# Kernel optimization log

Hardware: AMD Instinct MI355X
Metric: run time of the kernel (lower is better)

## Reference

```python
import jax, jax.numpy as jnp
import numpy as np

HEADS = 16
D_K = 64  # hidden_size // heads = 1024 // 16
SCALE = D_K ** 0.5


def setup_inputs() -> dict:
    key = jax.random.key(0)
    ks = jax.random.split(key, 7)
    B, S, D = 4, 2048, 1024
    H = 1024  # hidden_size
    O = 1024  # outputs_dims
    s = 0.02
    return {
        "query": jax.random.normal(ks[0], (B, S, D), dtype=jnp.float32),
        "key": jax.random.normal(ks[1], (B, S, D), dtype=jnp.float32),
        "value": jax.random.normal(ks[2], (B, S, D), dtype=jnp.float32),
        "Wq": jax.random.normal(ks[3], (D, H), dtype=jnp.float32) * s,
        "Wk": jax.random.normal(ks[4], (D, H), dtype=jnp.float32) * s,
        "Wv": jax.random.normal(ks[5], (D, H), dtype=jnp.float32) * s,
        "Wo": jax.random.normal(ks[6], (H, O), dtype=jnp.float32) * s,
    }


def reference(query, key, value, Wq, Wk, Wv, Wo):
    B, S, _ = query.shape
    # Dense projections with relu activation (as in the original module)
    q = jax.nn.relu(query @ Wq).reshape(B, S, HEADS, D_K)  # [B,S,H,dk]
    k = jax.nn.relu(key @ Wk).reshape(B, S, HEADS, D_K)
    v = jax.nn.relu(value @ Wv).reshape(B, S, HEADS, D_K)
    # scores: [B,H,Sq,Sk]
    scores = jnp.einsum('bqhd,bkhd->bhqk', q, k) / SCALE
    attn = jax.nn.softmax(scores, axis=-1)
    # attention-weighted values -> [B,Sq,H,dk] -> [B,Sq,H*dk]
    ctx = jnp.einsum('bhqk,bkhd->bqhd', attn, v).reshape(B, S, HEADS * D_K)
    out = jax.nn.relu(ctx @ Wo)
    return out
```

## Files before the change

kernel.cpp:

```cpp
#include <hip/hip_runtime.h>

typedef unsigned short u16;
typedef __bf16 bf16x8 __attribute__((ext_vector_type(8)));
typedef float f32x4 __attribute__((ext_vector_type(4)));
typedef u16 u16x8 __attribute__((ext_vector_type(8)));
typedef u16 u16x4 __attribute__((ext_vector_type(4)));

#define MFMA16(a, b, c) __builtin_amdgcn_mfma_f32_16x16x32_bf16(a, b, c, 0, 0, 0)

static constexpr float QSC = 0.18033688011112042f;

__device__ inline u16 f2bf(float f) {
  union { float f; unsigned u; } x; x.f = f;
  unsigned r = x.u + 0x7FFF + ((x.u >> 16) & 1);
  return (u16)(r >> 16);
}
__device__ inline u16 cvt_bf(float f) {
  __bf16 h = (__bf16)f; return __builtin_bit_cast(u16, h);
}
__device__ inline bf16x8 ld_frag(const u16* p) {
  return __builtin_bit_cast(bf16x8, *(const u16x8*)p);
}
__device__ inline void dma16(const u16* g, u16* l) {
  __builtin_amdgcn_global_load_lds(
      (const __attribute__((address_space(1))) unsigned*)g,
      (__attribute__((address_space(3))) unsigned*)l, 16, 0, 0);
}

#if __has_builtin(__builtin_amdgcn_exp2f)
#define EXP2(x) __builtin_amdgcn_exp2f(x)
#else
#define EXP2(x) exp2f(x)
#endif

__launch_bounds__(256)
__global__ void prep_w(const float* __restrict__ Wq, const float* __restrict__ Wk,
                       const float* __restrict__ Wv, const float* __restrict__ Wo,
                       u16* __restrict__ Wt) {
  __shared__ u16 T[64 * 72];
  const int z = blockIdx.z;
  const float* W = z == 0 ? Wq : z == 1 ? Wk : z == 2 ? Wv : Wo;
  u16* D = Wt + ((size_t)z << 20);
  const int k0 = blockIdx.y * 64, c0 = blockIdx.x * 64;
  const int tid = threadIdx.x;
  const int kr = tid >> 2, cs = (tid & 3) * 16;
  const float* src = W + (size_t)(k0 + kr) * 1024 + c0 + cs;
  float f[16];
#pragma unroll
  for (int i = 0; i < 4; ++i) *(float4*)&f[i * 4] = ((const float4*)src)[i];
#pragma unroll
  for (int i = 0; i < 16; ++i) T[(cs + i) * 72 + kr] = cvt_bf(f[i]);
  __syncthreads();
  const int nn = tid >> 2, ks = (tid & 3) * 16;
  u16* dst = D + (size_t)(c0 + nn) * 1024 + k0 + ks;
  *(u16x8*)dst = *(u16x8*)&T[nn * 72 + ks];
  *(u16x8*)(dst + 8) = *(u16x8*)&T[nn * 72 + ks + 8];
}

__launch_bounds__(256)
__global__ void prep_a(const float* __restrict__ q, const float* __restrict__ k,
                       const float* __restrict__ v, u16* __restrict__ dq,
                       u16* __restrict__ dk, u16* __restrict__ dv) {
  const int z = blockIdx.z;
  const float* s = z == 0 ? q : z == 1 ? k : v;
  u16* d = z == 0 ? dq : z == 1 ? dk : dv;
  for (size_t i = blockIdx.x * 256 + threadIdx.x; i < (size_t)1048576; i += 262144) {
    const float* g = s + i * 8;
    float4 f0 = *(const float4*)g, f1 = *(const float4*)(g + 4);
    u16x8 h;
    h[0] = cvt_bf(f0.x); h[1] = cvt_bf(f0.y); h[2] = cvt_bf(f0.z); h[3] = cvt_bf(f0.w);
    h[4] = cvt_bf(f1.x); h[5] = cvt_bf(f1.y); h[6] = cvt_bf(f1.z); h[7] = cvt_bf(f1.w);
    *(u16x8*)(d + i * 8) = h;
  }
}

__launch_bounds__(256, 3)
__global__ void gemm_fwd(const u16* __restrict__ Aq, const u16* __restrict__ Ak,
                         const u16* __restrict__ Av, const u16* __restrict__ Wt,
                         u16* __restrict__ Qw, u16* __restrict__ Kw,
                         u16* __restrict__ Vw) {
  __shared__ u16 smem[24576];
  const int z = blockIdx.z;
  const u16* A = z == 0 ? Aq : z == 1 ? Ak : Av;
  const u16* Bt = Wt + ((size_t)z << 20);
  u16* out = z == 0 ? Qw : z == 1 ? Kw : Vw;

  const int tid = threadIdx.x;
  const int lane = tid & 63, l15 = lane & 15, quad = lane >> 4;
  const int wv = tid >> 6, wm = wv & 1, wn = wv >> 1;
  const int m0 = (blockIdx.x * 8 + (blockIdx.y >> 3)) * 128;
  const int n0 = (blockIdx.y & 7) * 128;

  const int c0 = tid, c1 = 256 + tid;
  const u16* ga0 = A + (size_t)(m0 + (c0 & 127)) * 1024 + (c0 >> 7) * 8;
  const u16* ga1 = A + (size_t)(m0 + (c1 & 127)) * 1024 + (c1 >> 7) * 8;
  const u16* gb0 = Bt + (size_t)(n0 + (c0 & 127)) * 1024 + (c0 >> 7) * 8;
  const u16* gb1 = Bt + (size_t)(n0 + (c1 & 127)) * 1024 + (c1 >> 7) * 8;
  const int la0 = (wv * 64) * 8, la1 = (256 + wv * 64) * 8;

  f32x4 acc[4][4] = {};

#define STAGE(kt, bo)                                   \
  do {                                                  \
    const int k0_ = (kt) * 32;                          \
    dma16(ga0 + k0_, &smem[(bo) + la0]);                \
    dma16(gb0 + k0_, &smem[(bo) + 4096 + la0]);         \
    dma16(ga1 + k0_, &smem[(bo) + la1]);                \
    dma16(gb1 + k0_, &smem[(bo) + 4096 + la1]);         \
  } while (0)

  STAGE(0, 0);
  STAGE(1, 8192);
  asm volatile("s_waitcnt vmcnt(4)" ::: "memory");
  __builtin_amdgcn_sched_barrier(0);
  __builtin_amdgcn_s_barrier();

  int bo0 = 0, bo1 = 8192, bo2 = 16384;
  const int offA = (quad * 128 + wm * 64 + l15) * 8;
  const int offB = (quad * 128 + wn * 64 + l15) * 8;
#pragma unroll 1
  for (int t = 0; t < 32; ++t) {
    if (t < 30) STAGE(t + 2, bo2);
    const u16* Ab = smem + bo0;
    const u16* Bb = smem + bo0 + 4096;
    bf16x8 a[4], b[4];
#pragma unroll
    for (int i = 0; i < 4; ++i) a[i] = ld_frag(Ab + offA + i * 128);
#pragma unroll
    for (int j = 0; j < 4; ++j) b[j] = ld_frag(Bb + offB + j * 128);
    if (t < 30)
      asm volatile("s_waitcnt vmcnt(4) lgkmcnt(0)" ::: "memory");
    else
      asm volatile("s_waitcnt vmcnt(0) lgkmcnt(0)" ::: "memory");
    __builtin_amdgcn_sched_barrier(0);
    __builtin_amdgcn_s_barrier();
#pragma unroll
    for (int i = 0; i < 4; ++i)
#pragma unroll
      for (int j = 0; j < 4; ++j)
        acc[i][j] = MFMA16(a[i], b[j], acc[i][j]);
    const int tb = bo0; bo0 = bo1; bo1 = bo2; bo2 = tb;
  }
#undef STAGE

  if (z < 2) {
    const float sc = z == 0 ? QSC : 1.0f;
#pragma unroll
    for (int i = 0; i < 4; ++i)
#pragma unroll
      for (int j = 0; j < 4; ++j)
#pragma unroll
        for (int r = 0; r < 4; ++r) {
          float v = fmaxf(acc[i][j][r], 0.f) * sc;
          int m = m0 + wm * 64 + i * 16 + quad * 4 + r;
          int n = n0 + wn * 64 + j * 16 + l15;
          out[(size_t)m * 1024 + n] = f2bf(v);
        }
  } else {
    const int b = m0 >> 11, s0 = m0 & 2047;
#pragma unroll
    for (int half = 0; half < 2; ++half) {
      __syncthreads();
      if (wn == half) {
#pragma unroll
        for (int i = 0; i < 4; ++i)
#pragma unroll
          for (int j = 0; j < 4; ++j) {
            u16x4 pk;
#pragma unroll
            for (int r = 0; r < 4; ++r) pk[r] = f2bf(fmaxf(acc[i][j][r], 0.f));
            const int nn = j * 16 + l15;
            const int ml = wm * 64 + i * 16 + quad * 4;
            *(u16x4*)&smem[nn * 136 + ml] = pk;
          }
      }
      __syncthreads();
      const int h = (n0 + half * 64) >> 6;
      const int nn = tid >> 2, seg = (tid & 3) * 32;
      u16* dst = out + ((size_t)((b * 16 + h) * 64 + nn)) * 2048 + s0 + seg;
#pragma unroll
      for (int i2 = 0; i2 < 4; ++i2)
        *(u16x8*)&dst[i2 * 8] = *(u16x8*)&smem[nn * 136 + seg + i2 * 8];
    }
  }
}

__launch_bounds__(256, 3)
__global__ void gemm_out(const u16* __restrict__ A, const u16* __restrict__ Bt,
                         float* __restrict__ out) {
  __shared__ u16 smem[24576];
  const int tid = threadIdx.x;
  const int lane = tid & 63, l15 = lane & 15, quad = lane >> 4;
  const int wv = tid >> 6, wm = wv & 1, wn = wv >> 1;
  const int m0 = (blockIdx.x * 8 + (blockIdx.y >> 3)) * 128;
  const int n0 = (blockIdx.y & 7) * 128;

  const int c0 = tid, c1 = 256 + tid;
  const u16* ga0 = A + (size_t)(m0 + (c0 & 127)) * 1024 + (c0 >> 7) * 8;
  const u16* ga1 = A + (size_t)(m0 + (c1 & 127)) * 1024 + (c1 >> 7) * 8;
  const u16* gb0 = Bt + (size_t)(n0 + (c0 & 127)) * 1024 + (c0 >> 7) * 8;
  const u16* gb1 = Bt + (size_t)(n0 + (c1 & 127)) * 1024 + (c1 >> 7) * 8;
  const int la0 = (wv * 64) * 8, la1 = (256 + wv * 64) * 8;

  f32x4 acc[4][4] = {};

#define STAGE(kt, bo)                                   \
  do {                                                  \
    const int k0_ = (kt) * 32;                          \
    dma16(ga0 + k0_, &smem[(bo) + la0]);                \
    dma16(gb0 + k0_, &smem[(bo) + 4096 + la0]);         \
    dma16(ga1 + k0_, &smem[(bo) + la1]);                \
    dma16(gb1 + k0_, &smem[(bo) + 4096 + la1]);         \
  } while (0)

  STAGE(0, 0);
  STAGE(1, 8192);
  asm volatile("s_waitcnt vmcnt(4)" ::: "memory");
  __builtin_amdgcn_sched_barrier(0);
  __builtin_amdgcn_s_barrier();

  int bo0 = 0, bo1 = 8192, bo2 = 16384;
  const int offA = (quad * 128 + wm * 64 + l15) * 8;
  const int offB = (quad * 128 + wn * 64 + l15) * 8;
#pragma unroll 1
  for (int t = 0; t < 32; ++t) {
    if (t < 30) STAGE(t + 2, bo2);
    const u16* Ab = smem + bo0;
    const u16* Bb = smem + bo0 + 4096;
    bf16x8 a[4], b[4];
#pragma unroll
    for (int i = 0; i < 4; ++i) a[i] = ld_frag(Ab + offA + i * 128);
#pragma unroll
    for (int j = 0; j < 4; ++j) b[j] = ld_frag(Bb + offB + j * 128);
    if (t < 30)
      asm volatile("s_waitcnt vmcnt(4) lgkmcnt(0)" ::: "memory");
    else
      asm volatile("s_waitcnt vmcnt(0) lgkmcnt(0)" ::: "memory");
    __builtin_amdgcn_sched_barrier(0);
    __builtin_amdgcn_s_barrier();
#pragma unroll
    for (int i = 0; i < 4; ++i)
#pragma unroll
      for (int j = 0; j < 4; ++j)
        acc[i][j] = MFMA16(a[i], b[j], acc[i][j]);
    const int tb = bo0; bo0 = bo1; bo1 = bo2; bo2 = tb;
  }
#undef STAGE

#pragma unroll
  for (int i = 0; i < 4; ++i)
#pragma unroll
    for (int j = 0; j < 4; ++j)
#pragma unroll
      for (int r = 0; r < 4; ++r) {
        int m = m0 + wm * 64 + i * 16 + quad * 4 + r;
        int n = n0 + wn * 64 + j * 16 + l15;
        out[(size_t)m * 1024 + n] = fmaxf(acc[i][j][r], 0.f);
      }
}

__launch_bounds__(256, 3)
__global__ void attn(const u16* __restrict__ Q, const u16* __restrict__ K,
                     const u16* __restrict__ V, u16* __restrict__ ctx) {
  __shared__ u16 Ksm[2][4096];
  __shared__ u16 Vsm[2][4096];
  __shared__ u16 Psm[4][2048];

  const int tid = threadIdx.x;
  const int lane = tid & 63, l15 = lane & 15, quad = lane >> 4;
  const int wv = tid >> 6;
  const int bh = blockIdx.x, b = bh >> 4, h = bh & 15;
  const int q0 = blockIdx.y * 128 + wv * 32;

  const u16* Kb = K + ((size_t)b * 2048) * 1024 + h * 64;
  const u16* Vb = V + (size_t)bh * 64 * 2048;
  u16* Pw = Psm[wv];

  const int ck0 = tid, ck1 = 256 + tid;
  const u16* kg0 = Kb + (size_t)(ck0 & 63) * 1024 + (ck0 >> 6) * 8;
  const u16* kg1 = Kb + (size_t)(ck1 & 63) * 1024 + (ck1 >> 6) * 8;
  const u16* vg0 = Vb + (size_t)(ck0 & 63) * 2048 + (ck0 >> 6) * 8;
  const u16* vg1 = Vb + (size_t)(ck1 & 63) * 2048 + (ck1 >> 6) * 8;

  bf16x8 aq[2][2];
#pragma unroll
  for (int qh = 0; qh < 2; ++qh)
#pragma unroll
    for (int kk = 0; kk < 2; ++kk)
      aq[qh][kk] = ld_frag(Q + (size_t)(b * 2048 + q0 + qh * 16 + l15) * 1024 +
                           h * 64 + kk * 32 + quad * 8);

  f32x4 o[2][4] = {};
  float ls[2] = {0.f, 0.f};

  dma16(kg0, &Ksm[0][ck0 * 8]);
  dma16(kg1, &Ksm[0][ck1 * 8]);
  dma16(vg0, &Vsm[0][ck0 * 8]);
  dma16(vg1, &Vsm[0][ck1 * 8]);

#pragma unroll 1
  for (int t = 0; t < 32; ++t) {
    const int cur = t & 1, nxt = cur ^ 1;
    __syncthreads();

    if (t + 1 < 32) {
      const int kadv = (t + 1) * 64;
      dma16(kg0 + (size_t)kadv * 1024, &Ksm[nxt][ck0 * 8]);
      dma16(kg1 + (size_t)kadv * 1024, &Ksm[nxt][ck1 * 8]);
      dma16(vg0 + kadv, &Vsm[nxt][ck0 * 8]);
      dma16(vg1 + kadv, &Vsm[nxt][ck1 * 8]);
    }

    bf16x8 kf[2][4];
#pragma unroll
    for (int kk = 0; kk < 2; ++kk)
#pragma unroll
      for (int jj = 0; jj < 4; ++jj)
        kf[kk][jj] = ld_frag(&Ksm[cur][((kk * 4 + quad) * 64 + jj * 16 + l15) * 8]);

    f32x4 st[2][4] = {};
#pragma unroll
    for (int kk = 0; kk < 2; ++kk)
#pragma unroll
      for (int jj = 0; jj < 4; ++jj)
#pragma unroll
        for (int qh = 0; qh < 2; ++qh)
          st[qh][jj] = MFMA16(kf[kk][jj], aq[qh][kk], st[qh][jj]);

#pragma unroll
    for (int qh = 0; qh < 2; ++qh)
#pragma unroll
      for (int jj = 0; jj < 4; ++jj) {
        float p0 = EXP2(st[qh][jj][0]), p1 = EXP2(st[qh][jj][1]);
        float p2 = EXP2(st[qh][jj][2]), p3 = EXP2(st[qh][jj][3]);
        ls[qh] += (p0 + p1) + (p2 + p3);
        u16x4 pk;
        pk[0] = cvt_bf(p0); pk[1] = cvt_bf(p1);
        pk[2] = cvt_bf(p2); pk[3] = cvt_bf(p3);
        const int kc = jj * 2 + (quad >> 1);
        *(u16x4*)&Pw[(kc * 32 + qh * 16 + l15) * 8 + (quad & 1) * 4] = pk;
      }

#pragma unroll
    for (int kk = 0; kk < 2; ++kk) {
      bf16x8 pa[2];
#pragma unroll
      for (int qh = 0; qh < 2; ++qh)
        pa[qh] = ld_frag(&Pw[((kk * 4 + quad) * 32 + qh * 16 + l15) * 8]);
#pragma unroll
      for (int j = 0; j < 4; ++j) {
        bf16x8 vb = ld_frag(&Vsm[cur][((kk * 4 + quad) * 64 + j * 16 + l15) * 8]);
#pragma unroll
        for (int qh = 0; qh < 2; ++qh)
          o[qh][j] = MFMA16(vb, pa[qh], o[qh][j]);
      }
    }
  }

  float inv[2];
#pragma unroll
  for (int qh = 0; qh < 2; ++qh) {
    ls[qh] += __shfl_xor(ls[qh], 16, 64);
    ls[qh] += __shfl_xor(ls[qh], 32, 64);
    inv[qh] = 1.f / ls[qh];
  }

#pragma unroll
  for (int qh = 0; qh < 2; ++qh) {
    const int tok = b * 2048 + q0 + qh * 16 + l15;
#pragma unroll
    for (int j = 0; j < 4; ++j) {
      u16x4 pk;
#pragma unroll
      for (int r = 0; r < 4; ++r) pk[r] = cvt_bf(o[qh][j][r] * inv[qh]);
      *(u16x4*)&ctx[(size_t)tok * 1024 + h * 64 + j * 16 + quad * 4] = pk;
    }
  }
}

extern "C" void kernel_launch(void* const* d_in, const int* in_sizes, int n_in,
                              void* d_out, int out_size, void* d_ws, size_t ws_size,
                              hipStream_t stream) {
  const float* query = (const float*)d_in[0];
  const float* key   = (const float*)d_in[1];
  const float* value = (const float*)d_in[2];
  const float* Wq = (const float*)d_in[3];
  const float* Wk = (const float*)d_in[4];
  const float* Wv = (const float*)d_in[5];
  const float* Wo = (const float*)d_in[6];
  float* outp = (float*)d_out;

  u16* Wt  = (u16*)d_ws;
  u16* Awq = Wt + ((size_t)4 << 20);
  u16* Qw  = Awq + ((size_t)8 << 20);
  u16* Kw  = Qw + ((size_t)8 << 20);
  u16* Vt  = Kw + ((size_t)8 << 20);
  u16* Awk = (u16*)d_out;
  u16* Awv = Awk + ((size_t)8 << 20);
  u16* Cw  = Awq;

  prep_w<<<dim3(16, 16, 4), 256, 0, stream>>>(Wq, Wk, Wv, Wo, Wt);
  prep_a<<<dim3(1024, 1, 3), 256, 0, stream>>>(query, key, value, Awq, Awk, Awv);
  gemm_fwd<<<dim3(8, 64, 3), 256, 0, stream>>>(Awq, Awk, Awv, Wt, Qw, Kw, Vt);
  attn<<<dim3(64, 16), 256, 0, stream>>>(Qw, Kw, Vt, Cw);
  gemm_out<<<dim3(8, 64), 256, 0, stream>>>(Cw, Wt + ((size_t)3 << 20), outp);
}
```

Measured before the change: 401.5 us.

## Enlarge QKV projection GEMM tiles to 256x256 with 8 waves and swapped V operands

The QKV projection GEMM goes from 128x128 tiles with 4 waves and triple buffering to 256x256 tiles with 8 waves (512 threads) and a double-buffered, half-split DMA schedule. MFMA blocks are raised in priority with s_setprio. For V the operands are swapped so the transposed output is computed directly, and the transposed store goes through LDS without an explicit transpose. The aim is more data reuse per tile, higher MFMA density and less global traffic, at the cost of more register pressure, fewer blocks (384) and the loss of the deeper prefetch.

```diff
diff --git a/kernel.cpp b/kernel.cpp
--- a/kernel.cpp
+++ b/kernel.cpp
@@ -74,113 +74,135 @@
   }
 }
 
-__launch_bounds__(256, 3)
+__launch_bounds__(512, 4)
 __global__ void gemm_fwd(const u16* __restrict__ Aq, const u16* __restrict__ Ak,
                          const u16* __restrict__ Av, const u16* __restrict__ Wt,
                          u16* __restrict__ Qw, u16* __restrict__ Kw,
                          u16* __restrict__ Vw) {
-  __shared__ u16 smem[24576];
+  __shared__ u16 smem[32768];
   const int z = blockIdx.z;
   const u16* A = z == 0 ? Aq : z == 1 ? Ak : Av;
   const u16* Bt = Wt + ((size_t)z << 20);
   u16* out = z == 0 ? Qw : z == 1 ? Kw : Vw;
+  const u16* Aop = (z == 2) ? Bt : A;
+  const u16* Bop = (z == 2) ? A : Bt;
 
   const int tid = threadIdx.x;
   const int lane = tid & 63, l15 = lane & 15, quad = lane >> 4;
   const int wv = tid >> 6, wm = wv & 1, wn = wv >> 1;
-  const int m0 = (blockIdx.x * 8 + (blockIdx.y >> 3)) * 128;
-  const int n0 = (blockIdx.y & 7) * 128;
-
-  const int c0 = tid, c1 = 256 + tid;
-  const u16* ga0 = A + (size_t)(m0 + (c0 & 127)) * 1024 + (c0 >> 7) * 8;
-  const u16* ga1 = A + (size_t)(m0 + (c1 & 127)) * 1024 + (c1 >> 7) * 8;
-  const u16* gb0 = Bt + (size_t)(n0 + (c0 & 127)) * 1024 + (c0 >> 7) * 8;
-  const u16* gb1 = Bt + (size_t)(n0 + (c1 & 127)) * 1024 + (c1 >> 7) * 8;
-  const int la0 = (wv * 64) * 8, la1 = (256 + wv * 64) * 8;
-
-  f32x4 acc[4][4] = {};
-
-#define STAGE(kt, bo)                                   \
-  do {                                                  \
-    const int k0_ = (kt) * 32;                          \
-    dma16(ga0 + k0_, &smem[(bo) + la0]);                \
-    dma16(gb0 + k0_, &smem[(bo) + 4096 + la0]);         \
-    dma16(ga1 + k0_, &smem[(bo) + la1]);                \
-    dma16(gb1 + k0_, &smem[(bo) + 4096 + la1]);         \
-  } while (0)
-
-  STAGE(0, 0);
-  STAGE(1, 8192);
-  asm volatile("s_waitcnt vmcnt(4)" ::: "memory");
+  const int mblk = ((blockIdx.x & 7) << 2) | (blockIdx.x >> 3);
+  const int m0 = (z == 2) ? blockIdx.y * 256 : mblk * 256;
+  const int n0 = (z == 2) ? mblk * 256 : blockIdx.y * 256;
+
+  const int cA0 = tid, cA1 = 512 + tid;
+  const u16* gA0 = Aop + (size_t)(m0 + (cA0 & 255)) * 1024 + (cA0 >> 8) * 8;
+  const u16* gA1 = Aop + (size_t)(m0 + (cA1 & 255)) * 1024 + (cA1 >> 8) * 8;
+  const u16* gB0 = Bop + (size_t)(n0 + (cA0 & 255)) * 1024 + (cA0 >> 8) * 8;
+  const u16* gB1 = Bop + (size_t)(n0 + (cA1 & 255)) * 1024 + (cA1 >> 8) * 8;
+  const int ub0 = (wv * 64) * 8;
+  const int ub1 = (512 + wv * 64) * 8;
+
+  const int offA = (quad * 256 + wm * 128 + l15) * 8;
+  const int offB = 8192 + (quad * 256 + wn * 64 + l15) * 8;
+
+  f32x4 acc[8][4] = {};
+
+  dma16(gA0, &smem[ub0]);
+  dma16(gA1, &smem[ub1]);
+  dma16(gB0, &smem[8192 + ub0]);
+  dma16(gB1, &smem[8192 + ub1]);
+  asm volatile("s_waitcnt vmcnt(0)" ::: "memory");
   __builtin_amdgcn_sched_barrier(0);
   __builtin_amdgcn_s_barrier();
 
-  int bo0 = 0, bo1 = 8192, bo2 = 16384;
-  const int offA = (quad * 128 + wm * 64 + l15) * 8;
-  const int offB = (quad * 128 + wn * 64 + l15) * 8;
+#define STEP(bo, nbo, t)                                                      \
+  do {                                                                        \
+         \
+    if ((t) + 1 < 32) {                                                       \
+      dma16(gA0 + ((t) + 1) * 32, &smem[(nbo) + ub0]);                        \
+      dma16(gA1 + ((t) + 1) * 32, &smem[(nbo) + ub1]);                        \
+    }                                                                         \
+    bf16x8 a[4], b[4];                                                        \
+    _Pragma("unroll") for (int j = 0; j < 4; ++j)                             \
+        b[j] = ld_frag(&smem[(bo) + offB + j * 128]);                         \
+    _Pragma("unroll") for (int i = 0; i < 4; ++i)                             \
+        a[i] = ld_frag(&smem[(bo) + offA + i * 128]);                         \
+    asm volatile("s_waitcnt lgkmcnt(0)" ::: "memory");                        \
+    __builtin_amdgcn_sched_barrier(0);                                        \
+    __builtin_amdgcn_s_setprio(1);                                            \
+    _Pragma("unroll") for (int i = 0; i < 4; ++i)                             \
+        _Pragma("unroll") for (int j = 0; j < 4; ++j)                         \
+            acc[i][j] = MFMA16(a[i], b[j], acc[i][j]);                        \
+    __builtin_amdgcn_s_setprio(0);                                            \
+    __builtin_amdgcn_s_barrier();                                             \
+                  \
+    if ((t) + 1 < 32) {                                                       \
+      dma16(gB0 + ((t) + 1) * 32, &smem[(nbo) + 8192 + ub0]);                 \
+      dma16(gB1 + ((t) + 1) * 32, &smem[(nbo) + 8192 + ub1]);                 \
+    }                                                                         \
+    _Pragma("unroll") for (int i = 0; i < 4; ++i)                             \
+        a[i] = ld_frag(&smem[(bo) + offA + (4 + i) * 128]);                   \
+    asm volatile("s_waitcnt lgkmcnt(0)" ::: "memory");                        \
+    __builtin_amdgcn_sched_barrier(0);                                        \
+    __builtin_amdgcn_s_setprio(1);                                            \
+    _Pragma("unroll") for (int i = 0; i < 4; ++i)                             \
+        _Pragma("unroll") for (int j = 0; j < 4; ++j)                         \
+            acc[4 + i][j] = MFMA16(a[i], b[j], acc[4 + i][j]);                \
+    __builtin_amdgcn_s_setprio(0);                                            \
+        \
+    if ((t) + 1 < 32) {                                                       \
+      asm volatile("s_waitcnt vmcnt(0)" ::: "memory");                        \
+      __builtin_amdgcn_sched_barrier(0);                                      \
+    }                                                                         \
+    __builtin_amdgcn_s_barrier();                                             \
+  } while (0)
+
 #pragma unroll 1
-  for (int t = 0; t < 32; ++t) {
-    if (t < 30) STAGE(t + 2, bo2);
-    const u16* Ab = smem + bo0;
-    const u16* Bb = smem + bo0 + 4096;
-    bf16x8 a[4], b[4];
-#pragma unroll
-    for (int i = 0; i < 4; ++i) a[i] = ld_frag(Ab + offA + i * 128);
-#pragma unroll
-    for (int j = 0; j < 4; ++j) b[j] = ld_frag(Bb + offB + j * 128);
-    if (t < 30)
-      asm volatile("s_waitcnt vmcnt(4) lgkmcnt(0)" ::: "memory");
-    else
-      asm volatile("s_waitcnt vmcnt(0) lgkmcnt(0)" ::: "memory");
-    __builtin_amdgcn_sched_barrier(0);
-    __builtin_amdgcn_s_barrier();
-#pragma unroll
-    for (int i = 0; i < 4; ++i)
-#pragma unroll
-      for (int j = 0; j < 4; ++j)
-        acc[i][j] = MFMA16(a[i], b[j], acc[i][j]);
-    const int tb = bo0; bo0 = bo1; bo1 = bo2; bo2 = tb;
-  }
-#undef STAGE
+  for (int t2 = 0; t2 < 32; t2 += 2) {
+    STEP(0, 16384, t2);
+    STEP(16384, 0, t2 + 1);
+  }
+#undef STEP
 
   if (z < 2) {
     const float sc = z == 0 ? QSC : 1.0f;
 #pragma unroll
-    for (int i = 0; i < 4; ++i)
+    for (int i = 0; i < 8; ++i)
 #pragma unroll
       for (int j = 0; j < 4; ++j)
 #pragma unroll
         for (int r = 0; r < 4; ++r) {
           float v = fmaxf(acc[i][j][r], 0.f) * sc;
-          int m = m0 + wm * 64 + i * 16 + quad * 4 + r;
+          int m = m0 + wm * 128 + i * 16 + quad * 4 + r;
           int n = n0 + wn * 64 + j * 16 + l15;
           out[(size_t)m * 1024 + n] = f2bf(v);
         }
   } else {
-    const int b = m0 >> 11, s0 = m0 & 2047;
+    const int bb = n0 >> 11, s0 = n0 & 2047;
 #pragma unroll
     for (int half = 0; half < 2; ++half) {
       __syncthreads();
-      if (wn == half) {
-#pragma unroll
-        for (int i = 0; i < 4; ++i)
-#pragma unroll
-          for (int j = 0; j < 4; ++j) {
-            u16x4 pk;
-#pragma unroll
-            for (int r = 0; r < 4; ++r) pk[r] = f2bf(fmaxf(acc[i][j][r], 0.f));
-            const int nn = j * 16 + l15;
-            const int ml = wm * 64 + i * 16 + quad * 4;
-            *(u16x4*)&smem[nn * 136 + ml] = pk;
-          }
+      if ((wn >> 1) == half) {
+#pragma unroll
+        for (int i = 0; i < 8; ++i)
+#pragma unroll
+          for (int j = 0; j < 4; ++j)
+#pragma unroll
+            for (int r = 0; r < 4; ++r) {
+              const int row = wm * 128 + i * 16 + quad * 4 + r;
+              const int col = (wn & 1) * 64 + j * 16 + l15;
+              smem[row * 128 + col] = f2bf(fmaxf(acc[i][j][r], 0.f));
+            }
       }
       __syncthreads();
-      const int h = (n0 + half * 64) >> 6;
-      const int nn = tid >> 2, seg = (tid & 3) * 32;
-      u16* dst = out + ((size_t)((b * 16 + h) * 64 + nn)) * 2048 + s0 + seg;
-#pragma unroll
-      for (int i2 = 0; i2 < 4; ++i2)
-        *(u16x8*)&dst[i2 * 8] = *(u16x8*)&smem[nn * 136 + seg + i2 * 8];
+#pragma unroll
+      for (int i2 = 0; i2 < 8; ++i2) {
+        const int c = i2 * 512 + tid;
+        const int row = c >> 4, ch = c & 15;
+        u16* dst = out + (size_t)(bb * 1024 + m0 + row) * 2048 + s0 +
+                   half * 128 + ch * 8;
+        *(u16x8*)dst = *(u16x8*)&smem[row * 128 + ch * 8];
+      }
     }
   }
 }
@@ -401,7 +423,7 @@
 
   prep_w<<<dim3(16, 16, 4), 256, 0, stream>>>(Wq, Wk, Wv, Wo, Wt);
   prep_a<<<dim3(1024, 1, 3), 256, 0, stream>>>(query, key, value, Awq, Awk, Awv);
-  gemm_fwd<<<dim3(8, 64, 3), 256, 0, stream>>>(Awq, Awk, Awv, Wt, Qw, Kw, Vt);
+  gemm_fwd<<<dim3(32, 4, 3), 512, 0, stream>>>(Awq, Awk, Awv, Wt, Qw, Kw, Vt);
   attn<<<dim3(64, 16), 256, 0, stream>>>(Qw, Kw, Vt, Cw);
   gemm_out<<<dim3(8, 64), 256, 0, stream>>>(Cw, Wt + ((size_t)3 << 20), outp);
 }
```

New measurement: 776.5 us. +93.4%, slower.
